# Kernel optimization log

Hardware: AMD Instinct MI355X
Metric: run time of the kernel (lower is better)

The kernel has to match this reference:

```python
import jax, jax.numpy as jnp
import numpy as np

NH = 8        # num_heads
KS = 64       # key_size
C_IN = 256
C_OUT = 3 * NH * KS   # 1536
GROUPS = 3 * NH       # 24
EPS = 1e-5
H = W = 64


def setup_inputs() -> dict:
    key = jax.random.key(0)
    k1, k2 = jax.random.split(key)
    x = jax.random.normal(k1, (1, C_IN, H, W), dtype=jnp.float32)
    conv_w = jax.random.normal(k2, (C_OUT, C_IN, 1, 1), dtype=jnp.float32) * 0.05
    gn_w = jnp.ones((C_OUT,), dtype=jnp.float32)
    gn_b = jnp.zeros((C_OUT,), dtype=jnp.float32)
    return {"x": x, "conv_w": conv_w, "gn_w": gn_w, "gn_b": gn_b}


def reference(x, conv_w, gn_w, gn_b):
    B, _, h, w = x.shape
    # 1x1 conv (normalize=True -> no bias): per-pixel GEMM over channels
    attn = jnp.einsum('bchw,oc->bohw', x, conv_w[:, :, 0, 0])  # [B, 1536, H, W]
    # GroupNorm: 24 groups of KS channels, normalized over (KS, H, W)
    g = attn.reshape(B, GROUPS, -1)
    mean = g.mean(axis=-1, keepdims=True)
    var = g.var(axis=-1, keepdims=True)
    g = (g - mean) * jax.lax.rsqrt(var + EPS)
    attn = g.reshape(B, C_OUT, h, w) * gn_w[None, :, None, None] + gn_b[None, :, None, None]
    # split into key, query, value (in that order, per chunk(3, dim=2))
    attn = attn.reshape(B, NH, 3 * KS, h * w)
    key_, query, value = jnp.split(attn, 3, axis=2)   # each [B, NH, KS, HW]
    # saliency = q^T @ k / sqrt(KS) -> [B, NH, HW, HW]
    saliency = jnp.einsum('bnkq,bnkl->bnql', query, key_) / jnp.sqrt(jnp.float32(KS))
    mask = jax.nn.softmax(saliency, axis=-1)
    # out = v @ mask^T -> [B, NH, KS, HW]
    out = jnp.einsum('bnkl,bnql->bnkq', value, mask)
    return out.reshape(B, NH * KS, h, w)
```

## Files before the change

### kernel.cpp

```cpp
#include <hip/hip_runtime.h>

typedef __bf16 bf16;
typedef __bf16 bf16x8 __attribute__((ext_vector_type(8)));
typedef __bf16 bf16x4 __attribute__((ext_vector_type(4)));
typedef float f32x4 __attribute__((ext_vector_type(4)));
typedef float f32x16 __attribute__((ext_vector_type(16)));


#define QF 0.18033688011112042f
#define EXPF(x) __builtin_amdgcn_exp2f(x)
#define MFMA32(A, B, C) __builtin_amdgcn_mfma_f32_32x32x16_bf16(A, B, C, 0, 0, 0)

union U4 { bf16x4 v; unsigned u[2]; };
union U8 { bf16x8 v; unsigned u[4]; };

__global__ void k_misc(const float* __restrict__ x, const float* __restrict__ w,
                       bf16* __restrict__ xT, bf16* __restrict__ wb, float* __restrict__ cs) {
    int b = blockIdx.x;
    if (b < 256) {
        __shared__ float ld[64][65];
        int cb = (b & 3) * 64;
        int pb = (b >> 2) * 64;
        int tp = (threadIdx.x & 15) * 4;
        int tc = threadIdx.x >> 4;
#pragma unroll
        for (int pass = 0; pass < 4; pass++) {
            int c = tc + pass * 16;
            float4 f = *(const float4*)(x + (cb + c) * 4096 + pb + tp);
            ld[tp][c] = f.x; ld[tp + 1][c] = f.y; ld[tp + 2][c] = f.z; ld[tp + 3][c] = f.w;
        }
        __syncthreads();
        int px = threadIdx.x >> 3;
        int co = (threadIdx.x & 7) * 8;
#pragma unroll
        for (int pass = 0; pass < 2; pass++) {
            int p2 = px + pass * 32;
            bf16x8 o;
#pragma unroll
            for (int j = 0; j < 8; j++) o[j] = (bf16)ld[p2][co + j];
            *(bf16x8*)(xT + (pb + p2) * 256 + cb + co) = o;
        }
    } else if (b < 640) {
        int idx = ((b - 256) * 256 + threadIdx.x) * 4;
        float4 f = *(const float4*)(w + idx);
        bf16x4 o;
        o[0] = (bf16)f.x; o[1] = (bf16)f.y; o[2] = (bf16)f.z; o[3] = (bf16)f.w;
        *(bf16x4*)(wb + idx) = o;
    } else {
#pragma unroll
        for (int i = 0; i < 12; i++) cs[i * 256 + threadIdx.x] = 0.f;
    }
}

__global__ __launch_bounds__(256) void k_conv(const bf16* __restrict__ Wb,
                                              const bf16* __restrict__ xT,
                                              bf16* __restrict__ qkvT,
                                              float* __restrict__ cs) {
    __shared__ __attribute__((aligned(16))) bf16 xs[64 * 72];
    __shared__ __attribute__((aligned(16))) bf16 ws2[64 * 72];
    int wid = threadIdx.x >> 6, lane = threadIdx.x & 63;
    int quad = lane >> 4, l15 = lane & 15;
    int g  = blockIdx.x % 24;
    int pb = (blockIdx.x / 24) * 64;
    int h = g / 3, sec = g % 3;
    int ob = g * 64;

    int srow = threadIdx.x >> 2;
    int scol = (threadIdx.x & 3) * 16;

    f32x4 acc[4];
#pragma unroll
    for (int c = 0; c < 4; c++) acc[c] = (f32x4){0.f, 0.f, 0.f, 0.f};

    bf16x8 fx0 = *(const bf16x8*)(xT + (pb + srow) * 256 + scol);
    bf16x8 fx1 = *(const bf16x8*)(xT + (pb + srow) * 256 + scol + 8);
    bf16x8 fw0 = *(const bf16x8*)(Wb + (ob + srow) * 256 + scol);
    bf16x8 fw1 = *(const bf16x8*)(Wb + (ob + srow) * 256 + scol + 8);

    for (int c4 = 0; c4 < 4; c4++) {
        __syncthreads();
        *(bf16x8*)(xs  + srow * 72 + scol)     = fx0;
        *(bf16x8*)(xs  + srow * 72 + scol + 8) = fx1;
        *(bf16x8*)(ws2 + srow * 72 + scol)     = fw0;
        *(bf16x8*)(ws2 + srow * 72 + scol + 8) = fw1;
        __syncthreads();

        if (c4 < 3) {
            int co = (c4 + 1) * 64;
            fx0 = *(const bf16x8*)(xT + (pb + srow) * 256 + co + scol);
            fx1 = *(const bf16x8*)(xT + (pb + srow) * 256 + co + scol + 8);
            fw0 = *(const bf16x8*)(Wb + (ob + srow) * 256 + co + scol);
            fw1 = *(const bf16x8*)(Wb + (ob + srow) * 256 + co + scol + 8);
        }

#pragma unroll
        for (int k2 = 0; k2 < 2; k2++) {
            bf16x8 a = *(const bf16x8*)(ws2 + (wid * 16 + l15) * 72 + k2 * 32 + quad * 8);
#pragma unroll
            for (int c = 0; c < 4; c++) {
                bf16x8 b = *(const bf16x8*)(xs + (c * 16 + l15) * 72 + k2 * 32 + quad * 8);
                acc[c] = __builtin_amdgcn_mfma_f32_16x16x32_bf16(a, b, acc[c], 0, 0, 0);
            }
        }
    }

    int ch0 = wid * 16 + quad * 4;
#pragma unroll
    for (int r = 0; r < 4; r++) {
        float sp  = acc[0][r] + acc[1][r] + acc[2][r] + acc[3][r];
        float ssp = acc[0][r] * acc[0][r] + acc[1][r] * acc[1][r]
                  + acc[2][r] * acc[2][r] + acc[3][r] * acc[3][r];
#pragma unroll
        for (int m = 1; m < 16; m <<= 1) {
            sp  += __shfl_xor(sp,  m, 64);
            ssp += __shfl_xor(ssp, m, 64);
        }
        if (l15 == 0) {
            atomicAdd(cs + (ob + ch0 + r) * 2,     sp);
            atomicAdd(cs + (ob + ch0 + r) * 2 + 1, ssp);
        }
    }

    __syncthreads();
    bf16* tile = xs;
    if (sec == 2) {
#pragma unroll
        for (int c = 0; c < 4; c++)
#pragma unroll
            for (int r = 0; r < 4; r++)
                tile[(ch0 + r) * 72 + c * 16 + l15] = (bf16)acc[c][r];
    } else {
#pragma unroll
        for (int c = 0; c < 4; c++) {
            bf16x4 o;
#pragma unroll
            for (int r = 0; r < 4; r++) o[r] = (bf16)acc[c][r];
            *(bf16x4*)(&tile[(c * 16 + l15) * 72 + ch0]) = o;
        }
    }
    __syncthreads();
    bf16* base = qkvT + h * 786432;
    int t = threadIdx.x;
    if (sec == 2) {
        bf16* V = base + 524288;
#pragma unroll
        for (int it = 0; it < 2; it++) {
            int e = it * 256 + t; int ch = e >> 3; int pxo = (e & 7) * 8;
            *(bf16x8*)(V + ch * 4096 + pb + pxo) = *(const bf16x8*)(&tile[ch * 72 + pxo]);
        }
    } else {
        bf16* dst = base + (sec == 0 ? 262144 : 0);
#pragma unroll
        for (int it = 0; it < 2; it++) {
            int e = it * 256 + t; int px = e >> 3; int cho = (e & 7) * 8;
            *(bf16x8*)(dst + (pb + px) * 64 + cho) = *(const bf16x8*)(&tile[px * 72 + cho]);
        }
    }
}

#define PF_BLOCK(S, LACC, PFA, PFB)                                             \
    {                                                                           \
        float p0 = EXPF(S[0]),  p1 = EXPF(S[1]),  p2 = EXPF(S[2]),  p3 = EXPF(S[3]);   \
        float p4 = EXPF(S[4]),  p5 = EXPF(S[5]),  p6 = EXPF(S[6]),  p7 = EXPF(S[7]);   \
        float p8 = EXPF(S[8]),  p9 = EXPF(S[9]),  p10 = EXPF(S[10]), p11 = EXPF(S[11]); \
        float p12 = EXPF(S[12]), p13 = EXPF(S[13]), p14 = EXPF(S[14]), p15 = EXPF(S[15]); \
        LACC += (((p0 + p1) + (p2 + p3)) + ((p4 + p5) + (p6 + p7)))             \
              + (((p8 + p9) + (p10 + p11)) + ((p12 + p13) + (p14 + p15)));      \
        U4 lo, hi;                                                              \
        lo.v[0] = (bf16)p0;  lo.v[1] = (bf16)p1;  lo.v[2] = (bf16)p2;  lo.v[3] = (bf16)p3;  \
        hi.v[0] = (bf16)p4;  hi.v[1] = (bf16)p5;  hi.v[2] = (bf16)p6;  hi.v[3] = (bf16)p7;  \
        unsigned a0 = lo.u[0], b0 = hi.u[0], a1 = lo.u[1], b1 = hi.u[1];        \
        asm("v_permlane32_swap_b32 %0, %1" : "+v"(a0), "+v"(b0));               \
        asm("v_permlane32_swap_b32 %0, %1" : "+v"(a1), "+v"(b1));               \
        U8 fA; fA.u[0] = a0; fA.u[1] = a1; fA.u[2] = b0; fA.u[3] = b1;          \
        PFA = fA.v;                                                             \
        U4 lo2, hi2;                                                            \
        lo2.v[0] = (bf16)p8;  lo2.v[1] = (bf16)p9;  lo2.v[2] = (bf16)p10; lo2.v[3] = (bf16)p11; \
        hi2.v[0] = (bf16)p12; hi2.v[1] = (bf16)p13; hi2.v[2] = (bf16)p14; hi2.v[3] = (bf16)p15; \
        unsigned a2 = lo2.u[0], b2 = hi2.u[0], a3 = lo2.u[1], b3 = hi2.u[1];    \
        asm("v_permlane32_swap_b32 %0, %1" : "+v"(a2), "+v"(b2));               \
        asm("v_permlane32_swap_b32 %0, %1" : "+v"(a3), "+v"(b3));               \
        U8 fB; fB.u[0] = a2; fB.u[1] = a3; fB.u[2] = b2; fB.u[3] = b3;          \
        PFB = fB.v;                                                             \
    }

#define STAGE(BK, BV)                                                           \
    *(bf16x8*)((BK) + r0 * 72 + koff)        = kf0;                             \
    *(bf16x8*)((BK) + (r0 + 32) * 72 + koff) = kf1;                             \
    *(bf16x8*)((BV) + r0 * 72 + koff)        = vf0;                             \
    *(bf16x8*)((BV) + (r0 + 32) * 72 + koff) = vf1;

#define PREFETCH(T)                                                             \
    {   int nb = (T) * 64;                                                      \
        kf0 = *(const bf16x8*)(KT + (nb + r0) * 64 + koff);                     \
        kf1 = *(const bf16x8*)(KT + (nb + r0 + 32) * 64 + koff);                \
        vf0 = *(const bf16x8*)(V + r0 * 4096 + nb + koff);                      \
        vf1 = *(const bf16x8*)(V + (r0 + 32) * 4096 + nb + koff); }

#define QK64(KSB)                                                               \
    {   const bf16* kra = (KSB) + l31 * 72 + half * 8;                          \
        const bf16* krb = (KSB) + (32 + l31) * 72 + half * 8;                   \
        s00 = (f32x16)(0.0f); s01 = (f32x16)(0.0f);                             \
        s10 = (f32x16)(0.0f); s11 = (f32x16)(0.0f);                             \
        __builtin_amdgcn_s_setprio(1);                                          \
        { bf16x8 fa = *(const bf16x8*)(kra +  0), fb = *(const bf16x8*)(krb +  0); \
          s00 = MFMA32(fa, bqA[0], s00); s01 = MFMA32(fa, bqB[0], s01);         \
          s10 = MFMA32(fb, bqA[0], s10); s11 = MFMA32(fb, bqB[0], s11); }       \
        { bf16x8 fa = *(const bf16x8*)(kra + 16), fb = *(const bf16x8*)(krb + 16); \
          s00 = MFMA32(fa, bqA[1], s00); s01 = MFMA32(fa, bqB[1], s01);         \
          s10 = MFMA32(fb, bqA[1], s10); s11 = MFMA32(fb, bqB[1], s11); }       \
        { bf16x8 fa = *(const bf16x8*)(kra + 32), fb = *(const bf16x8*)(krb + 32); \
          s00 = MFMA32(fa, bqA[2], s00); s01 = MFMA32(fa, bqB[2], s01);         \
          s10 = MFMA32(fb, bqA[2], s10); s11 = MFMA32(fb, bqB[2], s11); }       \
        { bf16x8 fa = *(const bf16x8*)(kra + 48), fb = *(const bf16x8*)(krb + 48); \
          s00 = MFMA32(fa, bqA[3], s00); s01 = MFMA32(fa, bqB[3], s01);         \
          s10 = MFMA32(fb, bqA[3], s10); s11 = MFMA32(fb, bqB[3], s11); }       \
        __builtin_amdgcn_s_setprio(0); }

#define PV64(VSB)                                                               \
    {   const bf16* vra = (VSB) + l31 * 72 + half * 8;                          \
        const bf16* vrb = (VSB) + (32 + l31) * 72 + half * 8;                   \
        __builtin_amdgcn_s_setprio(1);                                          \
        { bf16x8 fa = *(const bf16x8*)(vra +  0), fb = *(const bf16x8*)(vrb +  0); \
          oA0 = MFMA32(fa, pa0, oA0); oB0 = MFMA32(fa, pb0, oB0);               \
          oA1 = MFMA32(fb, pa0, oA1); oB1 = MFMA32(fb, pb0, oB1); }             \
        { bf16x8 fa = *(const bf16x8*)(vra + 16), fb = *(const bf16x8*)(vrb + 16); \
          oA0 = MFMA32(fa, pa1, oA0); oB0 = MFMA32(fa, pb1, oB0);               \
          oA1 = MFMA32(fb, pa1, oA1); oB1 = MFMA32(fb, pb1, oB1); }             \
        { bf16x8 fa = *(const bf16x8*)(vra + 32), fb = *(const bf16x8*)(vrb + 32); \
          oA0 = MFMA32(fa, pa2, oA0); oB0 = MFMA32(fa, pb2, oB0);               \
          oA1 = MFMA32(fb, pa2, oA1); oB1 = MFMA32(fb, pb2, oB1); }             \
        { bf16x8 fa = *(const bf16x8*)(vra + 48), fb = *(const bf16x8*)(vrb + 48); \
          oA0 = MFMA32(fa, pa3, oA0); oB0 = MFMA32(fa, pb3, oB0);               \
          oA1 = MFMA32(fb, pa3, oA1); oB1 = MFMA32(fb, pb3, oB1); }             \
        __builtin_amdgcn_s_setprio(0); }

#define SOFTMAX_ALL()                                                           \
    {   float la0 = ls0, la1 = ls1;                                             \
        PF_BLOCK(s00, la0, pa0, pa1);                                           \
        PF_BLOCK(s10, la0, pa2, pa3);                                           \
        PF_BLOCK(s01, la1, pb0, pb1);                                           \
        PF_BLOCK(s11, la1, pb2, pb3);                                           \
        ls0 = la0; ls1 = la1; }

__global__ __launch_bounds__(256, 2) void k_attn(const bf16* __restrict__ qkvT,
                                                 const float2* __restrict__ cs,
                                                 const float* __restrict__ gnw,
                                                 const float* __restrict__ gnb,
                                                 bf16* __restrict__ Opart,
                                                 float* __restrict__ Lsum) {
    int bid   = blockIdx.x;
    int h     = bid & 7;
    int qb    = (bid >> 3) & 15;
    int split = bid >> 7;
    int wid = threadIdx.x >> 6, lane = threadIdx.x & 63;
    int l31 = lane & 31, half = lane >> 5;
    const bf16* QT = qkvT + h * 786432;
    const bf16* KT = QT + 262144;
    const bf16* V  = QT + 524288;
    int qw = qb * 256 + wid * 64;

    __shared__ __attribute__((aligned(16))) bf16 Ks[2][64 * 72];
    __shared__ __attribute__((aligned(16))) bf16 Vs[2][64 * 72];

    int r0   = threadIdx.x >> 3;
    int koff = (threadIdx.x & 7) * 8;

    float2 vK = cs[(h * 3) * 64 + lane];
    float2 vQ = cs[(h * 3 + 1) * 64 + lane];
    float sK = vK.x, qK = vK.y, sQ = vQ.x, qQ = vQ.y;
#pragma unroll
    for (int m = 1; m < 64; m <<= 1) {
        sK += __shfl_xor(sK, m, 64); qK += __shfl_xor(qK, m, 64);
        sQ += __shfl_xor(sQ, m, 64); qQ += __shfl_xor(qQ, m, 64);
    }
    const float N = 262144.0f;
    float meanK = sK / N, invK = rsqrtf(qK / N - meanK * meanK + 1e-5f);
    float meanQ = sQ / N, invQ = rsqrtf(qQ / N - meanQ * meanQ + 1e-5f);

    bf16x8 bqA[4], bqB[4];
#pragma unroll
    for (int ks = 0; ks < 4; ks++) {
        bf16x8 rawA = *(const bf16x8*)(QT + (qw + l31) * 64 + ks * 16 + half * 8);
        bf16x8 rawB = *(const bf16x8*)(QT + (qw + 32 + l31) * 64 + ks * 16 + half * 8);
#pragma unroll
        for (int j = 0; j < 8; j++) {
            int c = ks * 16 + half * 8 + j;
            float gwq = gnw[h * 192 + 64 + c] * invQ;
            float bvq = (gnb[h * 192 + 64 + c] - meanQ * gwq) * QF;
            float avq = gwq * QF;
            float aKc = gnw[h * 192 + c] * invK;
            bqA[ks][j] = (bf16)(aKc * (avq * (float)rawA[j] + bvq));
            bqB[ks][j] = (bf16)(aKc * (avq * (float)rawB[j] + bvq));
        }
    }

    f32x16 oA0 = (f32x16)(0.0f), oA1 = (f32x16)(0.0f);
    f32x16 oB0 = (f32x16)(0.0f), oB1 = (f32x16)(0.0f);
    f32x16 s00, s01, s10, s11;
    bf16x8 pa0, pa1, pa2, pa3, pb0, pb1, pb2, pb3;
    float ls0 = 0.f, ls1 = 0.f;

    int t0 = split * 16, t1 = t0 + 16;

    bf16x8 kf0, kf1, vf0, vf1;
    PREFETCH(t0);

    STAGE(Ks[t0 & 1], Vs[t0 & 1]);
    __syncthreads();
    PREFETCH(t0 + 1);
    QK64(Ks[t0 & 1]);
    SOFTMAX_ALL();

    for (int lt = t0 + 1; lt < t1; lt++) {
        __syncthreads();
        STAGE(Ks[lt & 1], Vs[lt & 1]);
        __syncthreads();
        if (lt + 1 < t1) PREFETCH(lt + 1);
        QK64(Ks[lt & 1]);
        PV64(Vs[(lt - 1) & 1]);
        SOFTMAX_ALL();
    }
    PV64(Vs[(t1 - 1) & 1]);

    ls0 += __shfl_xor(ls0, 32, 64);
    ls1 += __shfl_xor(ls1, 32, 64);
    if (half == 0) {
        Lsum[split * 32768 + h * 4096 + qw + l31]      = ls0;
        Lsum[split * 32768 + h * 4096 + qw + 32 + l31] = ls1;
    }

    bf16* Ob = Opart + split * 2097152;
#pragma unroll
    for (int r = 0; r < 16; r++) {
        int kd = (r & 3) + 8 * (r >> 2) + 4 * half;
        Ob[(h * 64 + kd) * 4096 + qw + l31]           = (bf16)oA0[r];
        Ob[(h * 64 + 32 + kd) * 4096 + qw + l31]      = (bf16)oA1[r];
        Ob[(h * 64 + kd) * 4096 + qw + 32 + l31]      = (bf16)oB0[r];
        Ob[(h * 64 + 32 + kd) * 4096 + qw + 32 + l31] = (bf16)oB1[r];
    }
}

__global__ void k_final(const bf16* __restrict__ Opart, const float* __restrict__ Lsum,
                        const float2* __restrict__ cs, const float* __restrict__ gnw,
                        const float* __restrict__ gnb, float* __restrict__ out) {
    int gid = blockIdx.x * 256 + threadIdx.x;
    int row = gid >> 9;
    int c8  = (gid & 511) << 3;
    int h   = row >> 6;

    int g = h * 3 + 2;
    int c = threadIdx.x & 63;
    float2 v = cs[g * 64 + c];
    float s = v.x, ss = v.y;
#pragma unroll
    for (int m = 1; m < 64; m <<= 1) { s += __shfl_xor(s, m, 64); ss += __shfl_xor(ss, m, 64); }
    const float N = 262144.0f;
    float mean = s / N;
    float inv  = rsqrtf(ss / N - mean * mean + 1e-5f);
    int gi = h * 192 + 128 + (row & 63);
    float gw = gnw[gi];
    float va = inv * gw;
    float vb = gnb[gi] - mean * inv * gw;

    float o[8] = {0, 0, 0, 0, 0, 0, 0, 0};
    float l[8] = {0, 0, 0, 0, 0, 0, 0, 0};
#pragma unroll
    for (int sp = 0; sp < 4; sp++) {
        bf16x8 vv = *(const bf16x8*)(Opart + sp * 2097152 + row * 4096 + c8);
        const float* L = Lsum + sp * 32768 + h * 4096 + c8;
        float4 l0 = *(const float4*)L;
        float4 l1 = *(const float4*)(L + 4);
#pragma unroll
        for (int j = 0; j < 8; j++) o[j] += (float)vv[j];
        l[0] += l0.x; l[1] += l0.y; l[2] += l0.z; l[3] += l0.w;
        l[4] += l1.x; l[5] += l1.y; l[6] += l1.z; l[7] += l1.w;
    }
    float4 r0, r1;
    r0.x = va * o[0] / l[0] + vb; r0.y = va * o[1] / l[1] + vb;
    r0.z = va * o[2] / l[2] + vb; r0.w = va * o[3] / l[3] + vb;
    r1.x = va * o[4] / l[4] + vb; r1.y = va * o[5] / l[5] + vb;
    r1.z = va * o[6] / l[6] + vb; r1.w = va * o[7] / l[7] + vb;
    *(float4*)(out + row * 4096 + c8)     = r0;
    *(float4*)(out + row * 4096 + c8 + 4) = r1;
}

extern "C" void kernel_launch(void* const* d_in, const int* in_sizes, int n_in,
                              void* d_out, int out_size, void* d_ws, size_t ws_size,
                              hipStream_t stream) {
    const float* x      = (const float*)d_in[0];
    const float* conv_w = (const float*)d_in[1];
    const float* gn_w   = (const float*)d_in[2];
    const float* gn_b   = (const float*)d_in[3];
    float* out = (float*)d_out;
    char* ws = (char*)d_ws;

    bf16*   qkvT  = (bf16*) (ws);
    bf16*   Opart = (bf16*) (ws + 12582912);
    bf16*   Wb    = (bf16*) (ws + 12582912);
    bf16*   xT    = (bf16*) (ws + 13369344);
    float*  Lsum  = (float*)(ws + 29360128);
    float*  cs    = (float*)(ws + 29884416);

    hipLaunchKernelGGL(k_misc,  dim3(641),  dim3(256), 0, stream, x, conv_w, xT, Wb, cs);
    hipLaunchKernelGGL(k_conv,  dim3(1536), dim3(256), 0, stream, Wb, xT, qkvT, cs);
    hipLaunchKernelGGL(k_attn,  dim3(512),  dim3(256), 0, stream, qkvT, (const float2*)cs,
                       gn_w, gn_b, Opart, Lsum);
    hipLaunchKernelGGL(k_final, dim3(1024), dim3(256), 0, stream, Opart, Lsum, (const float2*)cs, gn_w, gn_b, out);
}
```

Baseline: 130.1 us.

## Enlarge conv tile to 256 pixels per block to reuse weights

The 1x1 conv kernel now processes 256 pixels per block instead of 64, with each wave computing a 64x64 output tile (16 MFMAs per k-step) and reusing the weight fragments across four pixel sub-tiles. Grid shrinks from 1536 to 384 blocks. This reduces redundant weight loads and LDS traffic per MFMA, but raises register use (64 accumulator floats plus 8 prefetch vectors) and cuts the number of blocks, so occupancy and parallelism on a 256-CU part drop. The conv is only one of four kernels, so the effect on the total is limited.

```diff
diff --git a/kernel.cpp b/kernel.cpp
--- a/kernel.cpp
+++ b/kernel.cpp
@@ -10,6 +10,7 @@
 #define QF 0.18033688011112042f
 #define EXPF(x) __builtin_amdgcn_exp2f(x)
 #define MFMA32(A, B, C) __builtin_amdgcn_mfma_f32_32x32x16_bf16(A, B, C, 0, 0, 0)
+#define MFMA16(A, B, C) __builtin_amdgcn_mfma_f32_16x16x32_bf16(A, B, C, 0, 0, 0)
 
 union U4 { bf16x4 v; unsigned u[2]; };
 union U8 { bf16x8 v; unsigned u[4]; };
@@ -56,86 +57,104 @@
                                               const bf16* __restrict__ xT,
                                               bf16* __restrict__ qkvT,
                                               float* __restrict__ cs) {
-    __shared__ __attribute__((aligned(16))) bf16 xs[64 * 72];
+    __shared__ __attribute__((aligned(16))) bf16 xs[256 * 72];
     __shared__ __attribute__((aligned(16))) bf16 ws2[64 * 72];
     int wid = threadIdx.x >> 6, lane = threadIdx.x & 63;
     int quad = lane >> 4, l15 = lane & 15;
     int g  = blockIdx.x % 24;
-    int pb = (blockIdx.x / 24) * 64;
+    int pb = (blockIdx.x / 24) * 256;
     int h = g / 3, sec = g % 3;
     int ob = g * 64;
 
-    int srow = threadIdx.x >> 2;
-    int scol = (threadIdx.x & 3) * 16;
-
-    f32x4 acc[4];
-#pragma unroll
-    for (int c = 0; c < 4; c++) acc[c] = (f32x4){0.f, 0.f, 0.f, 0.f};
-
-    bf16x8 fx0 = *(const bf16x8*)(xT + (pb + srow) * 256 + scol);
-    bf16x8 fx1 = *(const bf16x8*)(xT + (pb + srow) * 256 + scol + 8);
-    bf16x8 fw0 = *(const bf16x8*)(Wb + (ob + srow) * 256 + scol);
-    bf16x8 fw1 = *(const bf16x8*)(Wb + (ob + srow) * 256 + scol + 8);
+    int xrr = threadIdx.x >> 3;
+    int xcc = (threadIdx.x & 7) * 8;
+    int swr = threadIdx.x >> 2;
+    int swc = (threadIdx.x & 3) * 16;
+
+    f32x4 acc[4][4];
+#pragma unroll
+    for (int c = 0; c < 4; c++)
+#pragma unroll
+        for (int p = 0; p < 4; p++) acc[c][p] = (f32x4){0.f, 0.f, 0.f, 0.f};
+
+    bf16x8 px[8], pw0, pw1;
+#pragma unroll
+    for (int pass = 0; pass < 8; pass++)
+        px[pass] = *(const bf16x8*)(xT + (pb + pass * 32 + xrr) * 256 + xcc);
+    pw0 = *(const bf16x8*)(Wb + (ob + swr) * 256 + swc);
+    pw1 = *(const bf16x8*)(Wb + (ob + swr) * 256 + swc + 8);
 
     for (int c4 = 0; c4 < 4; c4++) {
         __syncthreads();
-        *(bf16x8*)(xs  + srow * 72 + scol)     = fx0;
-        *(bf16x8*)(xs  + srow * 72 + scol + 8) = fx1;
-        *(bf16x8*)(ws2 + srow * 72 + scol)     = fw0;
-        *(bf16x8*)(ws2 + srow * 72 + scol + 8) = fw1;
+#pragma unroll
+        for (int pass = 0; pass < 8; pass++)
+            *(bf16x8*)(xs + (pass * 32 + xrr) * 72 + xcc) = px[pass];
+        *(bf16x8*)(ws2 + swr * 72 + swc)     = pw0;
+        *(bf16x8*)(ws2 + swr * 72 + swc + 8) = pw1;
         __syncthreads();
 
         if (c4 < 3) {
             int co = (c4 + 1) * 64;
-            fx0 = *(const bf16x8*)(xT + (pb + srow) * 256 + co + scol);
-            fx1 = *(const bf16x8*)(xT + (pb + srow) * 256 + co + scol + 8);
-            fw0 = *(const bf16x8*)(Wb + (ob + srow) * 256 + co + scol);
-            fw1 = *(const bf16x8*)(Wb + (ob + srow) * 256 + co + scol + 8);
+#pragma unroll
+            for (int pass = 0; pass < 8; pass++)
+                px[pass] = *(const bf16x8*)(xT + (pb + pass * 32 + xrr) * 256 + co + xcc);
+            pw0 = *(const bf16x8*)(Wb + (ob + swr) * 256 + co + swc);
+            pw1 = *(const bf16x8*)(Wb + (ob + swr) * 256 + co + swc + 8);
         }
 
 #pragma unroll
         for (int k2 = 0; k2 < 2; k2++) {
-            bf16x8 a = *(const bf16x8*)(ws2 + (wid * 16 + l15) * 72 + k2 * 32 + quad * 8);
-#pragma unroll
-            for (int c = 0; c < 4; c++) {
-                bf16x8 b = *(const bf16x8*)(xs + (c * 16 + l15) * 72 + k2 * 32 + quad * 8);
-                acc[c] = __builtin_amdgcn_mfma_f32_16x16x32_bf16(a, b, acc[c], 0, 0, 0);
+            bf16x8 a0 = *(const bf16x8*)(ws2 + (0 * 16 + l15) * 72 + k2 * 32 + quad * 8);
+            bf16x8 a1 = *(const bf16x8*)(ws2 + (1 * 16 + l15) * 72 + k2 * 32 + quad * 8);
+            bf16x8 a2 = *(const bf16x8*)(ws2 + (2 * 16 + l15) * 72 + k2 * 32 + quad * 8);
+            bf16x8 a3 = *(const bf16x8*)(ws2 + (3 * 16 + l15) * 72 + k2 * 32 + quad * 8);
+#pragma unroll
+            for (int p = 0; p < 4; p++) {
+                bf16x8 b = *(const bf16x8*)(xs + (wid * 64 + p * 16 + l15) * 72 + k2 * 32 + quad * 8);
+                acc[0][p] = MFMA16(a0, b, acc[0][p]);
+                acc[1][p] = MFMA16(a1, b, acc[1][p]);
+                acc[2][p] = MFMA16(a2, b, acc[2][p]);
+                acc[3][p] = MFMA16(a3, b, acc[3][p]);
             }
         }
     }
 
-    int ch0 = wid * 16 + quad * 4;
+#pragma unroll
+    for (int c = 0; c < 4; c++)
 #pragma unroll
     for (int r = 0; r < 4; r++) {
-        float sp  = acc[0][r] + acc[1][r] + acc[2][r] + acc[3][r];
-        float ssp = acc[0][r] * acc[0][r] + acc[1][r] * acc[1][r]
-                  + acc[2][r] * acc[2][r] + acc[3][r] * acc[3][r];
+        float sp  = acc[c][0][r] + acc[c][1][r] + acc[c][2][r] + acc[c][3][r];
+        float ssp = acc[c][0][r] * acc[c][0][r] + acc[c][1][r] * acc[c][1][r]
+                  + acc[c][2][r] * acc[c][2][r] + acc[c][3][r] * acc[c][3][r];
 #pragma unroll
         for (int m = 1; m < 16; m <<= 1) {
             sp  += __shfl_xor(sp,  m, 64);
             ssp += __shfl_xor(ssp, m, 64);
         }
         if (l15 == 0) {
-            atomicAdd(cs + (ob + ch0 + r) * 2,     sp);
-            atomicAdd(cs + (ob + ch0 + r) * 2 + 1, ssp);
+            atomicAdd(cs + (ob + c * 16 + quad * 4 + r) * 2,     sp);
+            atomicAdd(cs + (ob + c * 16 + quad * 4 + r) * 2 + 1, ssp);
         }
     }
 
     __syncthreads();
-    bf16* tile = xs;
     if (sec == 2) {
 #pragma unroll
         for (int c = 0; c < 4; c++)
 #pragma unroll
-            for (int r = 0; r < 4; r++)
-                tile[(ch0 + r) * 72 + c * 16 + l15] = (bf16)acc[c][r];
+        for (int p = 0; p < 4; p++)
+#pragma unroll
+        for (int r = 0; r < 4; r++)
+            xs[(c * 16 + quad * 4 + r) * 264 + wid * 64 + p * 16 + l15] = (bf16)acc[c][p][r];
     } else {
 #pragma unroll
-        for (int c = 0; c < 4; c++) {
+        for (int c = 0; c < 4; c++)
+#pragma unroll
+        for (int p = 0; p < 4; p++) {
             bf16x4 o;
 #pragma unroll
-            for (int r = 0; r < 4; r++) o[r] = (bf16)acc[c][r];
-            *(bf16x4*)(&tile[(c * 16 + l15) * 72 + ch0]) = o;
+            for (int r = 0; r < 4; r++) o[r] = (bf16)acc[c][p][r];
+            *(bf16x4*)(&xs[(wid * 64 + p * 16 + l15) * 72 + c * 16 + quad * 4]) = o;
         }
     }
     __syncthreads();
@@ -144,16 +163,20 @@
     if (sec == 2) {
         bf16* V = base + 524288;
 #pragma unroll
-        for (int it = 0; it < 2; it++) {
-            int e = it * 256 + t; int ch = e >> 3; int pxo = (e & 7) * 8;
-            *(bf16x8*)(V + ch * 4096 + pb + pxo) = *(const bf16x8*)(&tile[ch * 72 + pxo]);
+        for (int it = 0; it < 8; it++) {
+            int e = it * 256 + t;
+            int ch = e >> 5;
+            int pxo = (e & 31) * 8;
+            *(bf16x8*)(V + ch * 4096 + pb + pxo) = *(const bf16x8*)(&xs[ch * 264 + pxo]);
         }
     } else {
         bf16* dst = base + (sec == 0 ? 262144 : 0);
 #pragma unroll
-        for (int it = 0; it < 2; it++) {
-            int e = it * 256 + t; int px = e >> 3; int cho = (e & 7) * 8;
-            *(bf16x8*)(dst + (pb + px) * 64 + cho) = *(const bf16x8*)(&tile[px * 72 + cho]);
+        for (int it = 0; it < 8; it++) {
+            int e = it * 256 + t;
+            int pxw = e >> 3;
+            int cho = (e & 7) * 8;
+            *(bf16x8*)(dst + (pb + pxw) * 64 + cho) = *(const bf16x8*)(&xs[pxw * 72 + cho]);
         }
     }
 }
@@ -403,7 +426,7 @@
     float*  cs    = (float*)(ws + 29884416);
 
     hipLaunchKernelGGL(k_misc,  dim3(641),  dim3(256), 0, stream, x, conv_w, xT, Wb, cs);
-    hipLaunchKernelGGL(k_conv,  dim3(1536), dim3(256), 0, stream, Wb, xT, qkvT, cs);
+    hipLaunchKernelGGL(k_conv,  dim3(384),  dim3(256), 0, stream, Wb, xT, qkvT, cs);
     hipLaunchKernelGGL(k_attn,  dim3(512),  dim3(256), 0, stream, qkvT, (const float2*)cs,
                        gn_w, gn_b, Opart, Lsum);
     hipLaunchKernelGGL(k_final, dim3(1024), dim3(256), 0, stream, Opart, Lsum, (const float2*)cs, gn_w, gn_b, out);
```

New measurement: 141.6 us. 8.9% more time.
